# Optimization experiments

Measured on AMD Instinct MI355X. Metric: run time of the kernel, lower is better.

Reference implementation:

```python
import jax, jax.numpy as jnp
import numpy as np

P = 2        # patch size (all 3 dims)
NB = 8       # num_bands
N = 16       # d_state
DTR = 8      # dt_rank = d_model // 16
DCONV = 4    # d_conv
SMAX = 2.0   # smax_dt = smax_B = smax_C


def _ln(x, g, b):
    mu = x.mean(-1, keepdims=True)
    v = ((x - mu) ** 2).mean(-1, keepdims=True)
    return (x - mu) / jnp.sqrt(v + 1e-5) * g + b


def _silu(x):
    return x * jax.nn.sigmoid(x)


def _ssm_layer(x, band, m, rho, Win, bin_, convw, convb, Wx, Wdt, bdt, Alog, Dp,
               Wout, bout, edt, eB, eC, wr, wm):
    # x: [B, L, d_model] -> bidirectional conditioned selective scan (BiFCSSM)
    Bsz, L, _ = x.shape
    ED = convw.shape[0]
    xz = x @ Win + bin_
    xp, z = xz[..., :ED], xz[..., ED:]
    # depthwise causal conv1d over L
    xpad = jnp.pad(xp, ((0, 0), (DCONV - 1, 0), (0, 0)))
    xc = sum(xpad[:, k:k + L, :] * convw[:, k] for k in range(DCONV)) + convb
    xc = _silu(xc)
    dbl = xc @ Wx                                    # [B,L,DTR+2N]
    dt = jax.nn.softplus(dbl[..., :DTR] @ Wdt + bdt)  # [B,L,ED]
    # band/radius/mask conditioned modulation of delta, B, C
    s_dt = SMAX * jax.nn.sigmoid(edt[band][None] + wr[0] * rho[None] + wm[0] * m)
    s_B = SMAX * jax.nn.sigmoid(eB[band][None] + wr[1] * rho[None] + wm[1] * m)
    s_C = SMAX * jax.nn.sigmoid(eC[band][None] + wr[2] * rho[None] + wm[2] * m)
    dt = dt * s_dt[..., None]
    Bm = dbl[..., DTR:DTR + N] * s_B[..., None]       # [B,L,N]
    Cm = dbl[..., DTR + N:] * s_C[..., None]          # [B,L,N]
    A = -jnp.exp(Alog)                                # [ED,N]
    dA = jnp.exp(dt[..., None] * A)                   # [B,L,ED,N]
    dBu = (dA - 1.0) / A * Bm[:, :, None, :] * xc[..., None]   # exact ZOH
    dA_s = jnp.moveaxis(dA, 1, 0)
    dBu_s = jnp.moveaxis(dBu, 1, 0)
    C_s = jnp.moveaxis(Cm, 1, 0)
    h0 = jnp.zeros((Bsz, ED, N), x.dtype)

    def step(h, inp):
        a, bu, c = inp
        h = a * h + bu
        return h, jnp.einsum('ben,bn->be', h, c)

    _, yf = jax.lax.scan(step, h0, (dA_s, dBu_s, C_s))
    _, yb = jax.lax.scan(step, h0, (dA_s, dBu_s, C_s), reverse=True)
    y = jnp.moveaxis(yf + yb, 0, 1) + Dp * xc
    y = y * _silu(z)
    return y @ Wout + bout


def _fwd(kspace_ri, mask, pe_w, pe_b, pu_w, pu_b, ln_g, ln_b, fn_g, fn_b,
         cond_band, cond_rad_w, cond_mask_w, l0_Win, l0_bin, l0_convw, l0_convb,
         l0_Wx, l0_Wdt, l0_bdt, l0_Alog, l0_D, l0_Wout, l0_bout, l0_edt, l0_eB,
         l0_eC, l0_wr, l0_wm):
    Bsz, C, nx, ny, nz = kspace_ri.shape
    gx, gy, gz = nx // P, ny // P, nz // P
    L = gx * gy * gz
    # patch embed (Conv3d, kernel==stride) as blocked einsum
    xr = kspace_ri.reshape(Bsz, C, gx, P, gy, P, gz, P)
    x = jnp.einsum('bcxiyjzk,dcijk->bdxyz', xr, pe_w) + pe_b[None, :, None, None, None]
    DM = x.shape[1]
    x = x.reshape(Bsz, DM, L).transpose(0, 2, 1)               # [B,L,D]
    m = mask.reshape(Bsz, 1, gx, P, gy, P, gz, P).mean(axis=(3, 5, 7)).reshape(Bsz, L)
    m = jnp.clip(m, 0.0, 1.0)
    # raster scan ordering: identity permutation, rho_bar, band ids
    rho = jnp.arange(L, dtype=x.dtype) / float(L - 1)
    band = jnp.clip(jnp.floor(rho * NB).astype(jnp.int32), 0, NB - 1)
    # condition tokens
    cond = cond_band[band][None] + rho[None, :, None] * cond_rad_w + m[:, :, None] * cond_mask_w
    h = _ln(x + cond, ln_g, ln_b)
    h = h + _ssm_layer(_ln(h, fn_g, fn_b), band, m, rho, l0_Win, l0_bin, l0_convw,
                       l0_convb, l0_Wx, l0_Wdt, l0_bdt, l0_Alog, l0_D, l0_Wout,
                       l0_bout, l0_edt, l0_eB, l0_eC, l0_wr, l0_wm)
    # patch unembed (ConvTranspose3d, kernel==stride) as blocked einsum
    hg = h.transpose(0, 2, 1).reshape(Bsz, DM, gx, gy, gz)
    out = jnp.einsum('bdxyz,dcijk->bcxiyjzk', hg, pu_w).reshape(Bsz, C, nx, ny, nz)
    out = out + pu_b[None, :, None, None, None]
    return kspace_ri + out


def setup_inputs() -> dict:
    key = jax.random.key(0)
    ks = jax.random.split(key, 24)
    ED, DM, CIN = 256, 128, 16

    def nrm(k, shape, s):
        return jax.random.normal(k, shape, jnp.float32) * s

    return {
        'kspace_ri': jax.random.normal(ks[0], (1, CIN, 64, 64, 16), jnp.float32),
        'mask': jax.random.uniform(ks[1], (1, 1, 64, 64, 16), jnp.float32),
        'pe_w': nrm(ks[2], (DM, CIN, P, P, P), 0.09),
        'pe_b': nrm(ks[3], (DM,), 0.02),
        'pu_w': nrm(ks[4], (DM, CIN, P, P, P), 0.05),
        'pu_b': jnp.zeros((CIN,), jnp.float32),
        'ln_g': jnp.ones((DM,), jnp.float32),
        'ln_b': jnp.zeros((DM,), jnp.float32),
        'fn_g': jnp.ones((DM,), jnp.float32),
        'fn_b': jnp.zeros((DM,), jnp.float32),
        'cond_band': nrm(ks[5], (NB, DM), 0.02),
        'cond_rad_w': nrm(ks[6], (DM,), 0.02),
        'cond_mask_w': nrm(ks[7], (DM,), 0.02),
        'l0_Win': nrm(ks[8], (DM, 2 * ED), 0.05),
        'l0_bin': jnp.zeros((2 * ED,), jnp.float32),
        'l0_convw': nrm(ks[9], (ED, DCONV), 0.2),
        'l0_convb': jnp.zeros((ED,), jnp.float32),
        'l0_Wx': nrm(ks[10], (ED, DTR + 2 * N), 0.05),
        'l0_Wdt': nrm(ks[11], (DTR, ED), 0.1),
        'l0_bdt': jnp.full((ED,), -3.0, jnp.float32),
        'l0_Alog': jnp.log(jnp.tile(jnp.arange(1, N + 1, dtype=jnp.float32), (ED, 1))),
        'l0_D': jnp.ones((ED,), jnp.float32),
        'l0_Wout': nrm(ks[12], (ED, DM), 0.05),
        'l0_bout': jnp.zeros((DM,), jnp.float32),
        'l0_edt': nrm(ks[13], (NB,), 0.1),
        'l0_eB': nrm(ks[14], (NB,), 0.1),
        'l0_eC': nrm(ks[15], (NB,), 0.1),
        'l0_wr': nrm(ks[16], (3,), 0.1),
        'l0_wm': nrm(ks[17], (3,), 0.1),
    }


def reference(kspace_ri, mask, pe_w, pe_b, pu_w, pu_b, ln_g, ln_b, fn_g, fn_b,
              cond_band, cond_rad_w, cond_mask_w, l0_Win, l0_bin, l0_convw,
              l0_convb, l0_Wx, l0_Wdt, l0_bdt, l0_Alog, l0_D, l0_Wout, l0_bout,
              l0_edt, l0_eB, l0_eC, l0_wr, l0_wm):
    return _fwd(kspace_ri, mask, pe_w, pe_b, pu_w, pu_b, ln_g, ln_b, fn_g, fn_b,
                cond_band, cond_rad_w, cond_mask_w, l0_Win, l0_bin, l0_convw,
                l0_convb, l0_Wx, l0_Wdt, l0_bdt, l0_Alog, l0_D, l0_Wout, l0_bout,
                l0_edt, l0_eB, l0_eC, l0_wr, l0_wm)
```

## Files before the change

### kernel.cpp

```cpp
#include <hip/hip_runtime.h>
#include <hip/hip_bf16.h>

#define L_TOK 8192
#define NCh 512
#define CLh 16
#define NSEG 8
#define CPS (NCh / NSEG)
#define LOG2E 1.44269504088896f

typedef short bf16x8 __attribute__((ext_vector_type(8)));
typedef float f32x4 __attribute__((ext_vector_type(4)));

static __device__ __forceinline__ float nexp2(float x) {
#if __has_builtin(__builtin_amdgcn_exp2f)
    return __builtin_amdgcn_exp2f(x);
#else
    return exp2f(x);
#endif
}
static __device__ __forceinline__ float sigm(float x) {
    return 1.f / (1.f + nexp2(-x * LOG2E));
}
static __device__ __forceinline__ ushort f2bf(float x) {
    union { float f; uint u; } v; v.f = x;
    uint r = v.u + 0x7fffu + ((v.u >> 16) & 1u);
    return (ushort)(r >> 16);
}
static __device__ __forceinline__ float bf2f(ushort h) {
    union { float f; uint u; } v; v.u = ((uint)h) << 16;
    return v.f;
}
static __device__ __forceinline__ void f2hl(float x, ushort* hi, ushort* lo) {
    ushort h = f2bf(x);
    *hi = h;
    *lo = f2bf(x - bf2f(h));
}

#define W_PE   0
#define W_WIN  16384
#define W_WOUT 81920
#define W_PU   114688
#define W_PROJ 131072
#define W_TOT  212992

__global__ __launch_bounds__(256) void embed_ln_k(const float* __restrict__ ks,
                                                  const float* __restrict__ pe_w,
                                                  const float* __restrict__ Win,
                                                  const float* __restrict__ Wx, const float* __restrict__ Wdt,
                                                  const float* __restrict__ Wout, const float* __restrict__ pu_w,
                                                  const float* __restrict__ mask,
                                                  const float* __restrict__ pe_b, const float* __restrict__ cond_band,
                                                  const float* __restrict__ cond_rad, const float* __restrict__ cond_mask,
                                                  const float* __restrict__ ln_g, const float* __restrict__ ln_b,
                                                  const float* __restrict__ fn_g, const float* __restrict__ fn_b,
                                                  ushort* __restrict__ wH, ushort* __restrict__ wL,
                                                  float* __restrict__ mbuf,
                                                  float* __restrict__ h_,
                                                  ushort* __restrict__ hnH, ushort* __restrict__ hnL) {
    const int tid = threadIdx.x;
    if (blockIdx.x >= 512) {
        int b = blockIdx.x - 512;
        if (b >= 832) {
            int l = (b - 832) * 256 + tid;
            int xg = l >> 8, yg = (l >> 3) & 31, zg = l & 7;
            float s = 0.f;
            for (int i2 = 0; i2 < 2; ++i2)
                for (int j2 = 0; j2 < 2; ++j2)
                    for (int k2 = 0; k2 < 2; ++k2)
                        s += mask[(2 * xg + i2) * 1024 + (2 * yg + j2) * 16 + 2 * zg + k2];
            s *= 0.125f;
            mbuf[l] = fminf(fmaxf(s, 0.f), 1.f);
            return;
        }
        int i = b * 256 + tid;
        float v;
        if (i < 16384) {
            v = pe_w[i];
        } else if (i < 81920) {
            int j = i - 16384; int n = j >> 7, k = j & 127;
            v = Win[k * 512 + n];
        } else if (i < 114688) {
            int j = i - 81920; int n = j >> 8, k = j & 255;
            v = Wout[k * 128 + n];
        } else if (i < 131072) {
            int j = i - 114688; int n = j >> 7, k = j & 127;
            v = pu_w[k * 128 + n];
        } else {
            int j = i - 131072; int n = j >> 8, k = j & 255;
            if (n < 256) {
                float s = 0.f;
#pragma unroll
                for (int r = 0; r < 8; ++r) s += Wx[k * 40 + r] * Wdt[r * 256 + n];
                v = s;
            } else if (n < 288) {
                v = Wx[k * 40 + 8 + (n - 256)];
            } else {
                v = 0.f;
            }
        }
        ushort h, lo; f2hl(v, &h, &lo);
        wH[i] = h; wL[i] = lo;
        return;
    }

    __shared__ __align__(16) char smem[50176];
    __shared__ float mpool[16];
    ushort (*AsH)[72] = (ushort(*)[72])(smem);
    ushort (*AsL)[72] = (ushort(*)[72])(smem + 2304);
    ushort (*BsH)[72] = (ushort(*)[72])(smem + 4608);
    ushort (*BsL)[72] = (ushort(*)[72])(smem + 23040);
    float*  ksb       = (float*)(smem + 41472);
    float  (*Cs)[132] = (float(*)[132])(smem);

    const int lane = tid & 63, wn = tid >> 6;
    const int ln = lane & 15, q = lane >> 4;
    const int mb = blockIdx.x * 16;
    const int xg = mb >> 8, yg0 = (mb >> 3) & 31;

    for (int v = tid; v < 512; v += 256) {
        int seg = v >> 2, zq = v & 3;
        int cc = seg >> 3, i2 = (seg >> 2) & 1, yy = seg & 3;
        float4 t4 = *(const float4*)&ks[cc * 65536 + (2 * xg + i2) * 1024 + (2 * yg0 + yy) * 16 + zq * 4];
        int la = seg * 17 + zq * 4;
        ksb[la] = t4.x; ksb[la + 1] = t4.y; ksb[la + 2] = t4.z; ksb[la + 3] = t4.w;
    }
    if (tid < 16) {
        int l = mb + tid;
        int xg2 = l >> 8, yg2 = (l >> 3) & 31, zg2 = l & 7;
        float s = 0.f;
        for (int i2 = 0; i2 < 2; ++i2)
            for (int j2 = 0; j2 < 2; ++j2)
                for (int k2 = 0; k2 < 2; ++k2)
                    s += mask[(2 * xg2 + i2) * 1024 + (2 * yg2 + j2) * 16 + 2 * zg2 + k2];
        mpool[tid] = fminf(fmaxf(s * 0.125f, 0.f), 1.f);
    }

    f32x4 acc[2];
    acc[0] = (f32x4){0.f, 0.f, 0.f, 0.f};
    acc[1] = (f32x4){0.f, 0.f, 0.f, 0.f};

    for (int kc = 0; kc < 128; kc += 64) {
        __syncthreads();
        for (int u = tid; u < 1024; u += 256) {
            int r = u >> 6, kk = u & 63;
            int k = kc + kk;
            int cc = k >> 3, ijk = k & 7;
            int i2 = (ijk >> 2) & 1, j2 = (ijk >> 1) & 1, k2 = ijk & 1;
            int seg = (cc * 2 + i2) * 4 + (r >> 3) * 2 + j2;
            float v = ksb[seg * 17 + (r & 7) * 2 + k2];
            ushort hh, ll; f2hl(v, &hh, &ll);
            AsH[r][kk] = hh; AsL[r][kk] = ll;
        }
        for (int u = tid; u < 1024; u += 256) {
            int n = u >> 3, g = u & 7;
            const float* pw = &pe_w[n * 128 + kc + g * 8];
            float4 p0 = *(const float4*)pw;
            float4 p1 = *(const float4*)(pw + 4);
            union { ushort us[8]; uint4 v4; } hh, ll;
            f2hl(p0.x, &hh.us[0], &ll.us[0]); f2hl(p0.y, &hh.us[1], &ll.us[1]);
            f2hl(p0.z, &hh.us[2], &ll.us[2]); f2hl(p0.w, &hh.us[3], &ll.us[3]);
            f2hl(p1.x, &hh.us[4], &ll.us[4]); f2hl(p1.y, &hh.us[5], &ll.us[5]);
            f2hl(p1.z, &hh.us[6], &ll.us[6]); f2hl(p1.w, &hh.us[7], &ll.us[7]);
            *(uint4*)&BsH[n][g * 8] = hh.v4;
            *(uint4*)&BsL[n][g * 8] = ll.v4;
        }
        __syncthreads();
#pragma unroll
        for (int ks_ = 0; ks_ < 64; ks_ += 32) {
            const int kk = ks_ + q * 8;
            bf16x8 ah = *(const bf16x8*)&AsH[ln][kk];
            bf16x8 al = *(const bf16x8*)&AsL[ln][kk];
#pragma unroll
            for (int cb = 0; cb < 2; ++cb) {
                bf16x8 bh = *(const bf16x8*)&BsH[wn * 32 + cb * 16 + ln][kk];
                bf16x8 bl = *(const bf16x8*)&BsL[wn * 32 + cb * 16 + ln][kk];
                acc[cb] = __builtin_amdgcn_mfma_f32_16x16x32_bf16(ah, bh, acc[cb], 0, 0, 0);
                acc[cb] = __builtin_amdgcn_mfma_f32_16x16x32_bf16(ah, bl, acc[cb], 0, 0, 0);
                acc[cb] = __builtin_amdgcn_mfma_f32_16x16x32_bf16(al, bh, acc[cb], 0, 0, 0);
            }
        }
    }
    __syncthreads();
#pragma unroll
    for (int cb = 0; cb < 2; ++cb) {
#pragma unroll
        for (int r = 0; r < 4; ++r) {
            int row = q * 4 + r;
            int col = wn * 32 + cb * 16 + ln;
            int l = mb + row;
            float rho = (float)l * (1.0f / 8191.0f);
            int band = min(7, (int)(rho * 8.0f));
            Cs[row][col] = acc[cb][r] + pe_b[col] + cond_band[band * 128 + col]
                           + rho * cond_rad[col] + mpool[row] * cond_mask[col];
        }
    }
    __syncthreads();
    {
        int row = tid >> 4, j = tid & 15;
        int l = mb + row;
        float v8[8];
        float s = 0.f, s2 = 0.f;
#pragma unroll
        for (int i = 0; i < 8; ++i) {
            float v = Cs[row][j * 8 + i];
            v8[i] = v; s += v; s2 += v * v;
        }
#pragma unroll
        for (int o = 1; o < 16; o <<= 1) { s += __shfl_xor(s, o, 16); s2 += __shfl_xor(s2, o, 16); }
        float mu = s * (1.f / 128.f);
        float var = s2 * (1.f / 128.f) - mu * mu;
        float rstd = rsqrtf(fmaxf(var, 0.f) + 1e-5f);
        float hv[8];
        s = 0.f; s2 = 0.f;
#pragma unroll
        for (int i = 0; i < 8; ++i) {
            int col = j * 8 + i;
            float h = (v8[i] - mu) * rstd * ln_g[col] + ln_b[col];
            hv[i] = h; s += h; s2 += h * h;
        }
#pragma unroll
        for (int i = 0; i < 8; i += 4)
            *(float4*)&h_[(size_t)l * 128 + j * 8 + i] = make_float4(hv[i], hv[i + 1], hv[i + 2], hv[i + 3]);
#pragma unroll
        for (int o = 1; o < 16; o <<= 1) { s += __shfl_xor(s, o, 16); s2 += __shfl_xor(s2, o, 16); }
        mu = s * (1.f / 128.f);
        var = s2 * (1.f / 128.f) - mu * mu;
        rstd = rsqrtf(fmaxf(var, 0.f) + 1e-5f);
        union { ushort u[8]; uint4 v4; } oh, ol;
#pragma unroll
        for (int i = 0; i < 8; ++i) {
            int col = j * 8 + i;
            float o2 = (hv[i] - mu) * rstd * fn_g[col] + fn_b[col];
            ushort hh, ll; f2hl(o2, &hh, &ll);
            oh.u[i] = hh; ol.u[i] = ll;
        }
        *(uint4*)&hnH[(size_t)l * 128 + j * 8] = oh.v4;
        *(uint4*)&hnL[(size_t)l * 128 + j * 8] = ol.v4;
    }
}

__global__ __launch_bounds__(256) void win_k(const ushort* __restrict__ Ah, const ushort* __restrict__ Al,
                                             const ushort* __restrict__ wH, const ushort* __restrict__ wL,
                                             const float* __restrict__ bin_,
                                             float* __restrict__ xp, float* __restrict__ sz) {
    __shared__ ushort AsH[64][72], AsL[64][72];
    __shared__ ushort BsH[64][72], BsL[64][72];
    const int tid = threadIdx.x;
    const int lane = tid & 63, wave = tid >> 6;
    const int wm = wave & 1, wn = wave >> 1;
    const int ln = lane & 15, q = lane >> 4;
    const int mb = blockIdx.x * 64, nb = blockIdx.y * 64;

    f32x4 acc[2][2];
#pragma unroll
    for (int rb = 0; rb < 2; ++rb)
#pragma unroll
        for (int cb = 0; cb < 2; ++cb) acc[rb][cb] = (f32x4){0.f, 0.f, 0.f, 0.f};

    for (int kc = 0; kc < 128; kc += 64) {
        __syncthreads();
        for (int u = tid; u < 512; u += 256) {
            int r = u >> 3, g = u & 7;
            size_t go = (size_t)(mb + r) * 128 + kc + g * 8;
            *(uint4*)&AsH[r][g * 8] = *(const uint4*)&Ah[go];
            *(uint4*)&AsL[r][g * 8] = *(const uint4*)&Al[go];
        }
        for (int u = tid; u < 512; u += 256) {
            int n = u >> 3, g = u & 7;
            size_t go = (size_t)(W_WIN) + (size_t)(nb + n) * 128 + kc + g * 8;
            *(uint4*)&BsH[n][g * 8] = *(const uint4*)&wH[go];
            *(uint4*)&BsL[n][g * 8] = *(const uint4*)&wL[go];
        }
        __syncthreads();
#pragma unroll
        for (int ks_ = 0; ks_ < 64; ks_ += 32) {
            const int kk = ks_ + q * 8;
            bf16x8 ah[2], al[2], bh[2], bl[2];
#pragma unroll
            for (int rb = 0; rb < 2; ++rb) {
                ah[rb] = *(const bf16x8*)&AsH[wm * 32 + rb * 16 + ln][kk];
                al[rb] = *(const bf16x8*)&AsL[wm * 32 + rb * 16 + ln][kk];
            }
#pragma unroll
            for (int cb = 0; cb < 2; ++cb) {
                bh[cb] = *(const bf16x8*)&BsH[wn * 32 + cb * 16 + ln][kk];
                bl[cb] = *(const bf16x8*)&BsL[wn * 32 + cb * 16 + ln][kk];
            }
#pragma unroll
            for (int rb = 0; rb < 2; ++rb)
#pragma unroll
                for (int cb = 0; cb < 2; ++cb) {
                    acc[rb][cb] = __builtin_amdgcn_mfma_f32_16x16x32_bf16(ah[rb], bh[cb], acc[rb][cb], 0, 0, 0);
                    acc[rb][cb] = __builtin_amdgcn_mfma_f32_16x16x32_bf16(ah[rb], bl[cb], acc[rb][cb], 0, 0, 0);
                    acc[rb][cb] = __builtin_amdgcn_mfma_f32_16x16x32_bf16(al[rb], bh[cb], acc[rb][cb], 0, 0, 0);
                }
        }
    }
#pragma unroll
    for (int rb = 0; rb < 2; ++rb)
#pragma unroll
        for (int cb = 0; cb < 2; ++cb)
#pragma unroll
            for (int r = 0; r < 4; ++r) {
                int l = mb + wm * 32 + rb * 16 + q * 4 + r;
                int col = nb + wn * 32 + cb * 16 + ln;
                float v = acc[rb][cb][r] + bin_[col];
                if (col < 256) {
                    xp[(size_t)l * 256 + col] = v;
                } else {
                    sz[(size_t)l * 256 + (col - 256)] = v * sigm(v);
                }
            }
}

__global__ __launch_bounds__(512) void proj_k(const float* __restrict__ xp,
                                              const float* __restrict__ convw, const float* __restrict__ convb,
                                              const ushort* __restrict__ wH, const ushort* __restrict__ wL,
                                              const float* __restrict__ bdt, const float* __restrict__ mbuf,
                                              const float* __restrict__ edt, const float* __restrict__ eB,
                                              const float* __restrict__ eC, const float* __restrict__ wr,
                                              const float* __restrict__ wm,
                                              float* __restrict__ xc, float* __restrict__ dt,
                                              float* __restrict__ Bm, float* __restrict__ Cm) {
    __shared__ __align__(16) char smem[52224];
    ushort (*AsH)[264] = (ushort(*)[264])(smem);
    ushort (*AsL)[264] = (ushort(*)[264])(smem + 16896);
    ushort (*BsH)[72]  = (ushort(*)[72])(smem + 33792);
    ushort (*BsL)[72]  = (ushort(*)[72])(smem + 43008);
    const int tid = threadIdx.x;
    const int mb = blockIdx.x * 32;

    {
        const int cg = tid & 63;
        const int rg = tid >> 6;
        const int c0 = cg * 4;
        float4 cb4 = *(const float4*)&convb[c0];
        float4 cw0 = *(const float4*)&convw[(c0 + 0) * 4];
        float4 cw1 = *(const float4*)&convw[(c0 + 1) * 4];
        float4 cw2 = *(const float4*)&convw[(c0 + 2) * 4];
        float4 cw3 = *(const float4*)&convw[(c0 + 3) * 4];
        const int lbase = mb + rg * 4;
        float4 zero = make_float4(0.f, 0.f, 0.f, 0.f);
        float4 x0 = (lbase - 3 >= 0) ? *(const float4*)&xp[(size_t)(lbase - 3) * 256 + c0] : zero;
        float4 x1 = (lbase - 2 >= 0) ? *(const float4*)&xp[(size_t)(lbase - 2) * 256 + c0] : zero;
        float4 x2 = (lbase - 1 >= 0) ? *(const float4*)&xp[(size_t)(lbase - 1) * 256 + c0] : zero;
#pragma unroll
        for (int rr = 0; rr < 4; ++rr) {
            int l = lbase + rr;
            float4 x3 = *(const float4*)&xp[(size_t)l * 256 + c0];
            float o0 = cb4.x + x0.x * cw0.x + x1.x * cw0.y + x2.x * cw0.z + x3.x * cw0.w;
            float o1 = cb4.y + x0.y * cw1.x + x1.y * cw1.y + x2.y * cw1.z + x3.y * cw1.w;
            float o2 = cb4.z + x0.z * cw2.x + x1.z * cw2.y + x2.z * cw2.z + x3.z * cw2.w;
            float o3 = cb4.w + x0.w * cw3.x + x1.w * cw3.y + x2.w * cw3.z + x3.w * cw3.w;
            o0 *= sigm(o0); o1 *= sigm(o1); o2 *= sigm(o2); o3 *= sigm(o3);
            *(float4*)&xc[(size_t)l * 256 + c0] = make_float4(o0, o1, o2, o3);
            union { ushort u[4]; uint2 v2; } hh, ll;
            f2hl(o0, &hh.u[0], &ll.u[0]); f2hl(o1, &hh.u[1], &ll.u[1]);
            f2hl(o2, &hh.u[2], &ll.u[2]); f2hl(o3, &hh.u[3], &ll.u[3]);
            int row = l - mb;
            *(uint2*)&AsH[row][c0] = hh.v2;
            *(uint2*)&AsL[row][c0] = ll.v2;
            x0 = x1; x1 = x2; x2 = x3;
        }
    }
    const int pn = tid >> 3, pg = tid & 7;
    uint4 regH = *(const uint4*)&wH[(size_t)W_PROJ + (size_t)pn * 256 + pg * 8];
    uint4 regL = *(const uint4*)&wL[(size_t)W_PROJ + (size_t)pn * 256 + pg * 8];
    __syncthreads();

    const int lane = tid & 63, wave = tid >> 6;
    const int wm2 = wave & 1, wn4 = wave >> 1;
    const int ln = lane & 15, q = lane >> 4;
    for (int it = 0; it < 5; ++it) {
        int nb = it * 64;
        f32x4 acc = (f32x4){0.f, 0.f, 0.f, 0.f};
        for (int kci = 0; kci < 4; ++kci) {
            int kc = kci * 64;
            __syncthreads();
            *(uint4*)&BsH[pn][pg * 8] = regH;
            *(uint4*)&BsL[pn][pg * 8] = regL;
            int s = it * 4 + kci;
            if (s < 19) {
                int s2 = s + 1;
                int nb2 = (s2 >> 2) * 64, kc2 = (s2 & 3) * 64;
                size_t go = (size_t)W_PROJ + (size_t)(nb2 + pn) * 256 + kc2 + pg * 8;
                regH = *(const uint4*)&wH[go];
                regL = *(const uint4*)&wL[go];
            }
            __syncthreads();
#pragma unroll
            for (int ks_ = 0; ks_ < 64; ks_ += 32) {
                const int kka = kc + ks_ + q * 8;
                const int kkb = ks_ + q * 8;
                bf16x8 ah = *(const bf16x8*)&AsH[wm2 * 16 + ln][kka];
                bf16x8 al = *(const bf16x8*)&AsL[wm2 * 16 + ln][kka];
                bf16x8 bh = *(const bf16x8*)&BsH[wn4 * 16 + ln][kkb];
                bf16x8 bl = *(const bf16x8*)&BsL[wn4 * 16 + ln][kkb];
                acc = __builtin_amdgcn_mfma_f32_16x16x32_bf16(ah, bh, acc, 0, 0, 0);
                acc = __builtin_amdgcn_mfma_f32_16x16x32_bf16(ah, bl, acc, 0, 0, 0);
                acc = __builtin_amdgcn_mfma_f32_16x16x32_bf16(al, bh, acc, 0, 0, 0);
            }
        }
#pragma unroll
        for (int r = 0; r < 4; ++r) {
            int l = mb + wm2 * 16 + q * 4 + r;
            int col = nb + wn4 * 16 + ln;
            float v = acc[r];
            float rho = (float)l * (1.0f / 8191.0f);
            int band = min(7, (int)(rho * 8.0f));
            float mv = mbuf[l];
            if (col < 256) {
                float sc0 = 2.0f * sigm(edt[band] + wr[0] * rho + wm[0] * mv);
                float v2 = v + bdt[col];
                float sp = (v2 > 20.f) ? v2 : log1pf(expf(v2));
                dt[(size_t)l * 256 + col] = sp * sc0;
            } else if (col < 272) {
                float sc1 = 2.0f * sigm(eB[band] + wr[1] * rho + wm[1] * mv);
                Bm[(size_t)l * 16 + (col - 256)] = v * sc1;
            } else if (col < 288) {
                float sc2 = 2.0f * sigm(eC[band] + wr[2] * rho + wm[2] * mv);
                Cm[(size_t)l * 16 + (col - 272)] = v * sc2;
            }
        }
    }
}

__global__ __launch_bounds__(512) void scan0_k(const float* __restrict__ dt, const float* __restrict__ xc,
                                               const float* __restrict__ Bm, const float* __restrict__ Alog,
                                               float* __restrict__ Hb, float* __restrict__ sdtb) {
    const int c = blockIdx.x;
    const int tid = threadIdx.x;
    const int dir = tid >> 8, e = tid & 255;
    __shared__ float bms[CLh][16];
    for (int idx = tid; idx < CLh * 16; idx += 512)
        bms[idx >> 4][idx & 15] = Bm[c * (CLh * 16) + idx];
    float A2[16], iv[16], h[16];
#pragma unroll
    for (int n = 0; n < 16; ++n) {
        float ea = nexp2(Alog[e * 16 + n] * LOG2E);
        A2[n] = -ea * LOG2E;
        iv[n] = -1.0f / ea;
        h[n] = 0.f;
    }
    const int base = c * CLh;
    float cu[8], cx[8], nu[8], nx[8];
#pragma unroll
    for (int j = 0; j < 8; ++j) {
        int p = dir ? (CLh - 1 - j) : j;
        cu[j] = dt[(size_t)(base + p) * 256 + e];
        cx[j] = xc[(size_t)(base + p) * 256 + e];
    }
    __syncthreads();
    float sdt = 0.f;
#pragma unroll
    for (int g = 0; g < CLh / 8; ++g) {
        if (g + 1 < CLh / 8) {
#pragma unroll
            for (int j = 0; j < 8; ++j) {
                int s = (g + 1) * 8 + j;
                int p = dir ? (CLh - 1 - s) : s;
                nu[j] = dt[(size_t)(base + p) * 256 + e];
                nx[j] = xc[(size_t)(base + p) * 256 + e];
            }
        }
#pragma unroll
        for (int j = 0; j < 8; ++j) {
            float u = cu[j], xv = cx[j];
            int s = g * 8 + j;
            int p = dir ? (CLh - 1 - s) : s;
            union { float4 v[4]; float f[16]; } bb;
            const float4* bp = (const float4*)&bms[p][0];
            bb.v[0] = bp[0]; bb.v[1] = bp[1]; bb.v[2] = bp[2]; bb.v[3] = bp[3];
#pragma unroll
            for (int n = 0; n < 16; ++n) {
                float a = nexp2(A2[n] * u);
                float w = xv * bb.f[n] * iv[n];
                h[n] = a * (h[n] + w) - w;
            }
            sdt += u;
        }
#pragma unroll
        for (int j = 0; j < 8; ++j) { cu[j] = nu[j]; cx[j] = nx[j]; }
    }
    const size_t hofs = (size_t)(dir * NCh + c) * 4096 + e * 16;
#pragma unroll
    for (int j = 0; j < 4; ++j)
        *(float4*)&Hb[hofs + 4 * j] = make_float4(h[4 * j], h[4 * j + 1], h[4 * j + 2], h[4 * j + 3]);
    if (dir == 0) sdtb[c * 256 + e] = sdt;
}

__global__ __launch_bounds__(256) void combine1_k(const float* __restrict__ Hb, const float* __restrict__ sdtb,
                                                  const float* __restrict__ Alog,
                                                  float* __restrict__ Hpp, float* __restrict__ cumsdtb,
                                                  float* __restrict__ segq, float* __restrict__ segsdt) {
    const int gid = blockIdx.x * 256 + threadIdx.x;
    const int seg = gid >> 13;
    const int r = gid & 8191;
    const int d1 = r >> 12, en = r & 4095, e1 = en >> 4;
    const float A2e = -nexp2(Alog[en] * LOG2E) * LOG2E;
    float hi = 0.f, cum = 0.f;
    for (int k = 0; k < CPS; ++k) {
        const int pos = seg * CPS + k;
        const int c2 = d1 ? (NCh - 1 - pos) : pos;
        const size_t o2 = (size_t)(d1 * NCh + c2) * 4096 + en;
        const float sv = sdtb[c2 * 256 + e1];
        Hpp[o2] = hi;
        if ((en & 15) == 0) cumsdtb[(d1 * NCh + c2) * 256 + e1] = cum;
        hi = nexp2(A2e * sv) * hi + Hb[o2];
        cum += sv;
    }
    segq[(d1 * NSEG + seg) * 4096 + en] = hi;
    if ((en & 15) == 0) segsdt[(d1 * NSEG + seg) * 256 + e1] = cum;
}

__global__ __launch_bounds__(64) void combine2_k(const float* __restrict__ segq, const float* __restrict__ segsdt,
                                                 const float* __restrict__ Alog, float* __restrict__ segpre) {
    const int gid = blockIdx.x * 64 + threadIdx.x;
    const int d1 = gid >> 12, en = gid & 4095, e1 = en >> 4;
    const float A2e = -nexp2(Alog[en] * LOG2E) * LOG2E;
    float hi = 0.f;
#pragma unroll
    for (int s = 0; s < NSEG; ++s) {
        segpre[(d1 * NSEG + s) * 4096 + en] = hi;
        hi = nexp2(A2e * segsdt[(d1 * NSEG + s) * 256 + e1]) * hi + segq[(d1 * NSEG + s) * 4096 + en];
    }
}

template <int DIR>
static __device__ __forceinline__ void scan_dir(const float* __restrict__ dt, const float* __restrict__ xc,
                                                int base, int e,
                                                const float (*bms)[16], const float (*cms)[16],
                                                const float* A2, const float* iv,
                                                float* h, float* yreg, float* cxl) {
    float cu[8], cx[8], nu[8], nx[8];
#pragma unroll
    for (int j = 0; j < 8; ++j) {
        const int p = DIR ? (CLh - 1 - j) : j;
        cu[j] = dt[(size_t)(base + p) * 256 + e];
        cx[j] = xc[(size_t)(base + p) * 256 + e];
    }
#pragma unroll
    for (int g = 0; g < CLh / 8; ++g) {
        if (g + 1 < CLh / 8) {
#pragma unroll
            for (int j = 0; j < 8; ++j) {
                const int s = (g + 1) * 8 + j;
                const int p = DIR ? (CLh - 1 - s) : s;
                nu[j] = dt[(size_t)(base + p) * 256 + e];
                nx[j] = xc[(size_t)(base + p) * 256 + e];
            }
        }
#pragma unroll
        for (int j = 0; j < 8; ++j) {
            const int s = g * 8 + j;
            const int p = DIR ? (CLh - 1 - s) : s;
            float u = cu[j], xv = cx[j];
            union { float4 v[4]; float f[16]; } bb, cc;
            const float4* bp = (const float4*)&bms[p][0];
            bb.v[0] = bp[0]; bb.v[1] = bp[1]; bb.v[2] = bp[2]; bb.v[3] = bp[3];
            const float4* cp = (const float4*)&cms[p][0];
            cc.v[0] = cp[0]; cc.v[1] = cp[1]; cc.v[2] = cp[2]; cc.v[3] = cp[3];
            float y = 0.f;
#pragma unroll
            for (int n = 0; n < 16; ++n) {
                float a = nexp2(A2[n] * u);
                float w = xv * bb.f[n] * iv[n];
                h[n] = a * (h[n] + w) - w;
                y += h[n] * cc.f[n];
            }
            yreg[p] = y;
        }
#pragma unroll
        for (int j = 0; j < 8; ++j) { cu[j] = nu[j]; cx[j] = nx[j]; }
    }
#pragma unroll
    for (int j = 0; j < 8; ++j) cxl[j] = cx[j];
}

__global__ __launch_bounds__(512) void scan1g_k(const float* __restrict__ dt, const float* __restrict__ xc,
                                                const float* __restrict__ Bm, const float* __restrict__ Cm,
                                                const float* __restrict__ Alog,
                                                const float* __restrict__ Hpp, const float* __restrict__ cumsdtb,
                                                const float* __restrict__ segpre,
                                                const float* __restrict__ sz, const float* __restrict__ Dp,
                                                ushort* __restrict__ AHo, ushort* __restrict__ ALo) {
    const int c = blockIdx.x;
    const int tid = threadIdx.x;
    const int dir = tid >> 8;
    const int e = tid & 255;
    __shared__ float bms[CLh][16];
    __shared__ float cms[CLh][16];
    __shared__ float ysF[8][256];
    __shared__ float ysB[8][256];
    for (int idx = tid; idx < CLh * 16; idx += 512) {
        bms[idx >> 4][idx & 15] = Bm[c * (CLh * 16) + idx];
        cms[idx >> 4][idx & 15] = Cm[c * (CLh * 16) + idx];
    }
    float A2[16], iv[16], h[16];
#pragma unroll
    for (int n = 0; n < 16; ++n) {
        float ea = nexp2(Alog[e * 16 + n] * LOG2E);
        A2[n] = -ea * LOG2E;
        iv[n] = -1.0f / ea;
    }
    {
        const int pos = dir ? (NCh - 1 - c) : c;
        const int seg = pos / CPS;
        const float cum = cumsdtb[(dir * NCh + c) * 256 + e];
        const size_t hofs = (size_t)(dir * NCh + c) * 4096 + e * 16;
        const size_t so = (size_t)(dir * NSEG + seg) * 4096 + e * 16;
#pragma unroll
        for (int jj = 0; jj < 4; ++jj) {
            float4 hv = *(const float4*)&Hpp[hofs + 4 * jj];
            float4 sv = *(const float4*)&segpre[so + 4 * jj];
            h[4 * jj + 0] = hv.x + nexp2(A2[4 * jj + 0] * cum) * sv.x;
            h[4 * jj + 1] = hv.y + nexp2(A2[4 * jj + 1] * cum) * sv.y;
            h[4 * jj + 2] = hv.z + nexp2(A2[4 * jj + 2] * cum) * sv.z;
            h[4 * jj + 3] = hv.w + nexp2(A2[4 * jj + 3] * cum) * sv.w;
        }
    }
    const int base = c * CLh;
    float yreg[CLh], cxl[8];
    __syncthreads();
    if (dir == 0) {
        scan_dir<0>(dt, xc, base, e, bms, cms, A2, iv, h, yreg, cxl);
#pragma unroll
        for (int j = 0; j < 8; ++j) ysF[j][e] = yreg[j];
    } else {
        scan_dir<1>(dt, xc, base, e, bms, cms, A2, iv, h, yreg, cxl);
#pragma unroll
        for (int j = 0; j < 8; ++j) ysB[j][e] = yreg[8 + j];
    }
    __syncthreads();
    const float dpv = Dp[e];
    if (dir == 0) {
#pragma unroll
        for (int j = 0; j < 8; ++j) {
            const int l = 8 + j;
            size_t gl = (size_t)(base + l) * 256 + e;
            float a = (yreg[l] + ysB[j][e] + dpv * cxl[j]) * sz[gl];
            ushort hh, ll; f2hl(a, &hh, &ll);
            AHo[gl] = hh; ALo[gl] = ll;
        }
    } else {
#pragma unroll
        for (int j = 0; j < 8; ++j) {
            const int l = 7 - j;
            size_t gl = (size_t)(base + l) * 256 + e;
            float a = (ysF[l][e] + yreg[l] + dpv * cxl[j]) * sz[gl];
            ushort hh, ll; f2hl(a, &hh, &ll);
            AHo[gl] = hh; ALo[gl] = ll;
        }
    }
}

__global__ __launch_bounds__(512) void wu_k(const ushort* __restrict__ AH, const ushort* __restrict__ AL,
                                            const ushort* __restrict__ wH, const ushort* __restrict__ wL,
                                            const float* __restrict__ bout, const float* __restrict__ h_,
                                            const float* __restrict__ pu_b, const float* __restrict__ ks,
                                            float* __restrict__ out) {
    __shared__ __align__(16) char smem[70656];
    ushort (*AsH)[264] = (ushort(*)[264])(smem);
    ushort (*AsL)[264] = (ushort(*)[264])(smem + 16896);
    ushort (*BsH)[72]  = (ushort(*)[72])(smem + 33792);
    ushort (*BsL)[72]  = (ushort(*)[72])(smem + 52224);
    ushort (*hfH)[136] = (ushort(*)[136])(smem);
    ushort (*hfL)[136] = (ushort(*)[136])(smem + 8704);

    const int tid = threadIdx.x;
    const int lane = tid & 63, wave = tid >> 6;
    const int wm = wave & 1, wn = wave >> 1;
    const int ln = lane & 15, q = lane >> 4;
    const int mb = blockIdx.x * 32;

    for (int u = tid; u < 1024; u += 512) {
        int r = u >> 5, g = u & 31;
        size_t go = (size_t)(mb + r) * 256 + g * 8;
        *(uint4*)&AsH[r][g * 8] = *(const uint4*)&AH[go];
        *(uint4*)&AsL[r][g * 8] = *(const uint4*)&AL[go];
    }

    f32x4 acc[2];
    acc[0] = (f32x4){0.f, 0.f, 0.f, 0.f};
    acc[1] = (f32x4){0.f, 0.f, 0.f, 0.f};

    for (int kc = 0; kc < 256; kc += 64) {
        __syncthreads();
        for (int u = tid; u < 1024; u += 512) {
            int n = u >> 3, g = u & 7;
            size_t go = (size_t)(W_WOUT) + (size_t)n * 256 + kc + g * 8;
            *(uint4*)&BsH[n][g * 8] = *(const uint4*)&wH[go];
            *(uint4*)&BsL[n][g * 8] = *(const uint4*)&wL[go];
        }
        __syncthreads();
#pragma unroll
        for (int ks_ = 0; ks_ < 64; ks_ += 32) {
            const int kka = kc + ks_ + q * 8;
            const int kkb = ks_ + q * 8;
            bf16x8 ah = *(const bf16x8*)&AsH[wm * 16 + ln][kka];
            bf16x8 al = *(const bf16x8*)&AsL[wm * 16 + ln][kka];
#pragma unroll
            for (int cb = 0; cb < 2; ++cb) {
                bf16x8 bh = *(const bf16x8*)&BsH[wn * 32 + cb * 16 + ln][kkb];
                bf16x8 bl = *(const bf16x8*)&BsL[wn * 32 + cb * 16 + ln][kkb];
                acc[cb] = __builtin_amdgcn_mfma_f32_16x16x32_bf16(ah, bh, acc[cb], 0, 0, 0);
                acc[cb] = __builtin_amdgcn_mfma_f32_16x16x32_bf16(ah, bl, acc[cb], 0, 0, 0);
                acc[cb] = __builtin_amdgcn_mfma_f32_16x16x32_bf16(al, bh, acc[cb], 0, 0, 0);
            }
        }
    }
    __syncthreads();
#pragma unroll
    for (int cb = 0; cb < 2; ++cb)
#pragma unroll
        for (int r = 0; r < 4; ++r) {
            int row = wm * 16 + q * 4 + r;
            int col = wn * 32 + cb * 16 + ln;
            float v = acc[cb][r] + bout[col] + h_[(size_t)(mb + row) * 128 + col];
            ushort hh, ll; f2hl(v, &hh, &ll);
            hfH[row][col] = hh;
            hfL[row][col] = ll;
        }
    __syncthreads();

    f32x4 acc2[2];
    acc2[0] = (f32x4){0.f, 0.f, 0.f, 0.f};
    acc2[1] = (f32x4){0.f, 0.f, 0.f, 0.f};
    for (int kc = 0; kc < 128; kc += 64) {
        __syncthreads();
        for (int u = tid; u < 1024; u += 512) {
            int n = u >> 3, g = u & 7;
            size_t go = (size_t)(W_PU) + (size_t)n * 128 + kc + g * 8;
            *(uint4*)&BsH[n][g * 8] = *(const uint4*)&wH[go];
            *(uint4*)&BsL[n][g * 8] = *(const uint4*)&wL[go];
        }
        __syncthreads();
#pragma unroll
        for (int ks_ = 0; ks_ < 64; ks_ += 32) {
            const int kka = kc + ks_ + q * 8;
            const int kkb = ks_ + q * 8;
            bf16x8 ah = *(const bf16x8*)&hfH[wm * 16 + ln][kka];
            bf16x8 al = *(const bf16x8*)&hfL[wm * 16 + ln][kka];
#pragma unroll
            for (int cb = 0; cb < 2; ++cb) {
                bf16x8 bh = *(const bf16x8*)&BsH[wn * 32 + cb * 16 + ln][kkb];
                bf16x8 bl = *(const bf16x8*)&BsL[wn * 32 + cb * 16 + ln][kkb];
                acc2[cb] = __builtin_amdgcn_mfma_f32_16x16x32_bf16(ah, bh, acc2[cb], 0, 0, 0);
                acc2[cb] = __builtin_amdgcn_mfma_f32_16x16x32_bf16(ah, bl, acc2[cb], 0, 0, 0);
                acc2[cb] = __builtin_amdgcn_mfma_f32_16x16x32_bf16(al, bh, acc2[cb], 0, 0, 0);
            }
        }
    }
#pragma unroll
    for (int cb = 0; cb < 2; ++cb)
#pragma unroll
        for (int r = 0; r < 4; ++r) {
            int l = mb + wm * 16 + q * 4 + r;
            int col = wn * 32 + cb * 16 + ln;
            int xg = l >> 8, yg = (l >> 3) & 31, zg = l & 7;
            int cch = col >> 3, ijk = col & 7;
            int i2 = (ijk >> 2) & 1, j2 = (ijk >> 1) & 1, k2 = ijk & 1;
            size_t idx = (size_t)((cch * 64 + 2 * xg + i2) * 64 + (2 * yg + j2)) * 16 + 2 * zg + k2;
            out[idx] = acc2[cb][r] + pu_b[cch] + ks[idx];
        }
}

extern "C" void kernel_launch(void* const* d_in, const int* in_sizes, int n_in,
                              void* d_out, int out_size, void* d_ws, size_t ws_size,
                              hipStream_t stream) {
    const float* ks    = (const float*)d_in[0];
    const float* mask  = (const float*)d_in[1];
    const float* pe_w  = (const float*)d_in[2];
    const float* pe_b  = (const float*)d_in[3];
    const float* pu_w  = (const float*)d_in[4];
    const float* pu_b  = (const float*)d_in[5];
    const float* ln_g  = (const float*)d_in[6];
    const float* ln_b  = (const float*)d_in[7];
    const float* fn_g  = (const float*)d_in[8];
    const float* fn_b  = (const float*)d_in[9];
    const float* cond_band = (const float*)d_in[10];
    const float* cond_rad  = (const float*)d_in[11];
    const float* cond_mask = (const float*)d_in[12];
    const float* Win   = (const float*)d_in[13];
    const float* bin_  = (const float*)d_in[14];
    const float* convw = (const float*)d_in[15];
    const float* convb = (const float*)d_in[16];
    const float* Wx    = (const float*)d_in[17];
    const float* Wdt   = (const float*)d_in[18];
    const float* bdt   = (const float*)d_in[19];
    const float* Alog  = (const float*)d_in[20];
    const float* Dp    = (const float*)d_in[21];
    const float* Wout  = (const float*)d_in[22];
    const float* bout  = (const float*)d_in[23];
    const float* edt   = (const float*)d_in[24];
    const float* eB    = (const float*)d_in[25];
    const float* eC    = (const float*)d_in[26];
    const float* wr    = (const float*)d_in[27];
    const float* wm    = (const float*)d_in[28];
    float* out = (float*)d_out;

    char* base = (char*)d_ws;
    size_t o = 0;
    auto alloc = [&](size_t bytes) { char* p = base + o; o += (bytes + 255) & ~(size_t)255; return p; };
    float*  mbuf = (float*)alloc(32768);
    ushort* wH   = (ushort*)alloc(W_TOT * 2);
    ushort* wL   = (ushort*)alloc(W_TOT * 2);
    float*  h_   = (float*)alloc(4194304);
    ushort* hnH  = (ushort*)alloc(2097152);
    ushort* hnL  = (ushort*)alloc(2097152);
    float*  xp   = (float*)alloc(8388608);
    float*  sz   = (float*)alloc(8388608);
    float*  xc   = (float*)alloc(8388608);
    float*  dt   = (float*)alloc(8388608);
    float*  Bm   = (float*)alloc(524288);
    float*  Cm   = (float*)alloc(524288);
    float*  Hb   = (float*)alloc((size_t)2 * NCh * 4096 * 4);
    float*  Hpp  = (float*)alloc((size_t)2 * NCh * 4096 * 4);
    float*  sdtb = (float*)alloc((size_t)NCh * 256 * 4);
    float*  cumsdtb = (float*)alloc((size_t)2 * NCh * 256 * 4);
    float*  segq    = (float*)alloc((size_t)2 * NSEG * 4096 * 4);
    float*  segsdt  = (float*)alloc((size_t)2 * NSEG * 256 * 4);
    float*  segpre  = (float*)alloc((size_t)2 * NSEG * 4096 * 4);
    ushort* AHo  = (ushort*)alloc(4194304);
    ushort* ALo  = (ushort*)alloc(4194304);

    embed_ln_k<<<1376, 256, 0, stream>>>(ks, pe_w, Win, Wx, Wdt, Wout, pu_w, mask,
                                         pe_b, cond_band, cond_rad, cond_mask,
                                         ln_g, ln_b, fn_g, fn_b,
                                         wH, wL, mbuf, h_, hnH, hnL);
    win_k<<<dim3(128, 8), 256, 0, stream>>>(hnH, hnL, wH, wL, bin_, xp, sz);
    proj_k<<<256, 512, 0, stream>>>(xp, convw, convb, wH, wL, bdt, mbuf, edt, eB, eC, wr, wm,
                                    xc, dt, Bm, Cm);
    scan0_k<<<NCh, 512, 0, stream>>>(dt, xc, Bm, Alog, Hb, sdtb);
    combine1_k<<<256, 256, 0, stream>>>(Hb, sdtb, Alog, Hpp, cumsdtb, segq, segsdt);
    combine2_k<<<128, 64, 0, stream>>>(segq, segsdt, Alog, segpre);
    scan1g_k<<<NCh, 512, 0, stream>>>(dt, xc, Bm, Cm, Alog, Hpp, cumsdtb, segpre, sz, Dp, AHo, ALo);
    wu_k<<<256, 512, 0, stream>>>(AHo, ALo, wH, wL, bout, h_, pu_b, ks, out);
}
```

Measured before the change: 272.6 us.

## Compute local scan outputs in first pass and apply carry-in correction separately

The first chunk scan now also produces per-token local outputs y and cumulative dt sums and writes them to global buffers. The second chunk rescan is replaced by a fully parallel per-token kernel that adds the carry-in state contribution, C·exp(A·S)·h_prev, instead of re-running the recurrence. This removes the duplicated sequential scan work. In exchange it writes and reads two extra 16 MB buffers and recomputes exponentials for both directions per token.

After: 284.1 us. +4.2%, slower.

```diff
diff --git a/kernel.cpp b/kernel.cpp
--- a/kernel.cpp
+++ b/kernel.cpp
@@ -425,15 +425,20 @@
     }
 }
 
-__global__ __launch_bounds__(512) void scan0_k(const float* __restrict__ dt, const float* __restrict__ xc,
-                                               const float* __restrict__ Bm, const float* __restrict__ Alog,
-                                               float* __restrict__ Hb, float* __restrict__ sdtb) {
+__global__ __launch_bounds__(512) void scan0y_k(const float* __restrict__ dt, const float* __restrict__ xc,
+                                                const float* __restrict__ Bm, const float* __restrict__ Cm,
+                                                const float* __restrict__ Alog,
+                                                float* __restrict__ Hb, float* __restrict__ sdtb,
+                                                float* __restrict__ ybuf, float* __restrict__ sbuf) {
     const int c = blockIdx.x;
     const int tid = threadIdx.x;
     const int dir = tid >> 8, e = tid & 255;
     __shared__ float bms[CLh][16];
-    for (int idx = tid; idx < CLh * 16; idx += 512)
+    __shared__ float cms[CLh][16];
+    for (int idx = tid; idx < CLh * 16; idx += 512) {
         bms[idx >> 4][idx & 15] = Bm[c * (CLh * 16) + idx];
+        cms[idx >> 4][idx & 15] = Cm[c * (CLh * 16) + idx];
+    }
     float A2[16], iv[16], h[16];
 #pragma unroll
     for (int n = 0; n < 16; ++n) {
@@ -468,16 +473,23 @@
             float u = cu[j], xv = cx[j];
             int s = g * 8 + j;
             int p = dir ? (CLh - 1 - s) : s;
-            union { float4 v[4]; float f[16]; } bb;
+            union { float4 v[4]; float f[16]; } bb, cc;
             const float4* bp = (const float4*)&bms[p][0];
             bb.v[0] = bp[0]; bb.v[1] = bp[1]; bb.v[2] = bp[2]; bb.v[3] = bp[3];
+            const float4* cp = (const float4*)&cms[p][0];
+            cc.v[0] = cp[0]; cc.v[1] = cp[1]; cc.v[2] = cp[2]; cc.v[3] = cp[3];
+            float y = 0.f;
 #pragma unroll
             for (int n = 0; n < 16; ++n) {
                 float a = nexp2(A2[n] * u);
                 float w = xv * bb.f[n] * iv[n];
                 h[n] = a * (h[n] + w) - w;
+                y += h[n] * cc.f[n];
             }
             sdt += u;
+            size_t go = (size_t)(dir * L_TOK + base + p) * 256 + e;
+            ybuf[go] = y;
+            sbuf[go] = sdt;
         }
 #pragma unroll
         for (int j = 0; j < 8; ++j) { cu[j] = nu[j]; cx[j] = nx[j]; }
@@ -526,132 +538,57 @@
     }
 }
 
-template <int DIR>
-static __device__ __forceinline__ void scan_dir(const float* __restrict__ dt, const float* __restrict__ xc,
-                                                int base, int e,
-                                                const float (*bms)[16], const float (*cms)[16],
-                                                const float* A2, const float* iv,
-                                                float* h, float* yreg, float* cxl) {
-    float cu[8], cx[8], nu[8], nx[8];
-#pragma unroll
-    for (int j = 0; j < 8; ++j) {
-        const int p = DIR ? (CLh - 1 - j) : j;
-        cu[j] = dt[(size_t)(base + p) * 256 + e];
-        cx[j] = xc[(size_t)(base + p) * 256 + e];
-    }
-#pragma unroll
-    for (int g = 0; g < CLh / 8; ++g) {
-        if (g + 1 < CLh / 8) {
-#pragma unroll
-            for (int j = 0; j < 8; ++j) {
-                const int s = (g + 1) * 8 + j;
-                const int p = DIR ? (CLh - 1 - s) : s;
-                nu[j] = dt[(size_t)(base + p) * 256 + e];
-                nx[j] = xc[(size_t)(base + p) * 256 + e];
-            }
-        }
-#pragma unroll
-        for (int j = 0; j < 8; ++j) {
-            const int s = g * 8 + j;
-            const int p = DIR ? (CLh - 1 - s) : s;
-            float u = cu[j], xv = cx[j];
-            union { float4 v[4]; float f[16]; } bb, cc;
-            const float4* bp = (const float4*)&bms[p][0];
-            bb.v[0] = bp[0]; bb.v[1] = bp[1]; bb.v[2] = bp[2]; bb.v[3] = bp[3];
-            const float4* cp = (const float4*)&cms[p][0];
-            cc.v[0] = cp[0]; cc.v[1] = cp[1]; cc.v[2] = cp[2]; cc.v[3] = cp[3];
-            float y = 0.f;
-#pragma unroll
-            for (int n = 0; n < 16; ++n) {
-                float a = nexp2(A2[n] * u);
-                float w = xv * bb.f[n] * iv[n];
-                h[n] = a * (h[n] + w) - w;
-                y += h[n] * cc.f[n];
-            }
-            yreg[p] = y;
-        }
-#pragma unroll
-        for (int j = 0; j < 8; ++j) { cu[j] = nu[j]; cx[j] = nx[j]; }
-    }
-#pragma unroll
-    for (int j = 0; j < 8; ++j) cxl[j] = cx[j];
-}
-
-__global__ __launch_bounds__(512) void scan1g_k(const float* __restrict__ dt, const float* __restrict__ xc,
-                                                const float* __restrict__ Bm, const float* __restrict__ Cm,
-                                                const float* __restrict__ Alog,
-                                                const float* __restrict__ Hpp, const float* __restrict__ cumsdtb,
-                                                const float* __restrict__ segpre,
-                                                const float* __restrict__ sz, const float* __restrict__ Dp,
-                                                ushort* __restrict__ AHo, ushort* __restrict__ ALo) {
-    const int c = blockIdx.x;
-    const int tid = threadIdx.x;
-    const int dir = tid >> 8;
-    const int e = tid & 255;
-    __shared__ float bms[CLh][16];
-    __shared__ float cms[CLh][16];
-    __shared__ float ysF[8][256];
-    __shared__ float ysB[8][256];
-    for (int idx = tid; idx < CLh * 16; idx += 512) {
-        bms[idx >> 4][idx & 15] = Bm[c * (CLh * 16) + idx];
-        cms[idx >> 4][idx & 15] = Cm[c * (CLh * 16) + idx];
-    }
-    float A2[16], iv[16], h[16];
-#pragma unroll
-    for (int n = 0; n < 16; ++n) {
-        float ea = nexp2(Alog[e * 16 + n] * LOG2E);
-        A2[n] = -ea * LOG2E;
-        iv[n] = -1.0f / ea;
-    }
-    {
+__global__ __launch_bounds__(512) void final_k(const float* __restrict__ ybuf, const float* __restrict__ sbuf,
+                                               const float* __restrict__ xc, const float* __restrict__ sz,
+                                               const float* __restrict__ Cm, const float* __restrict__ Alog,
+                                               const float* __restrict__ Hpp, const float* __restrict__ cumsdtb,
+                                               const float* __restrict__ segpre, const float* __restrict__ Dp,
+                                               ushort* __restrict__ AHo, ushort* __restrict__ ALo) {
+    const int gid = blockIdx.x * 512 + threadIdx.x;
+    const int l = gid >> 8, e = gid & 255;
+    const int c = l >> 4;
+    union { float4 v[4]; float f[16]; } A2, cmv;
+#pragma unroll
+    for (int j = 0; j < 4; ++j) {
+        float4 av = *(const float4*)&Alog[e * 16 + 4 * j];
+        A2.f[4 * j + 0] = -nexp2(av.x * LOG2E) * LOG2E;
+        A2.f[4 * j + 1] = -nexp2(av.y * LOG2E) * LOG2E;
+        A2.f[4 * j + 2] = -nexp2(av.z * LOG2E) * LOG2E;
+        A2.f[4 * j + 3] = -nexp2(av.w * LOG2E) * LOG2E;
+        cmv.v[j] = *(const float4*)&Cm[l * 16 + 4 * j];
+    }
+    float corr[2];
+#pragma unroll
+    for (int dir = 0; dir < 2; ++dir) {
+        const int cidx = dir * NCh + c;
         const int pos = dir ? (NCh - 1 - c) : c;
         const int seg = pos / CPS;
-        const float cum = cumsdtb[(dir * NCh + c) * 256 + e];
-        const size_t hofs = (size_t)(dir * NCh + c) * 4096 + e * 16;
+        const float cum = cumsdtb[cidx * 256 + e];
+        const size_t hofs = (size_t)cidx * 4096 + e * 16;
         const size_t so = (size_t)(dir * NSEG + seg) * 4096 + e * 16;
-#pragma unroll
-        for (int jj = 0; jj < 4; ++jj) {
-            float4 hv = *(const float4*)&Hpp[hofs + 4 * jj];
-            float4 sv = *(const float4*)&segpre[so + 4 * jj];
-            h[4 * jj + 0] = hv.x + nexp2(A2[4 * jj + 0] * cum) * sv.x;
-            h[4 * jj + 1] = hv.y + nexp2(A2[4 * jj + 1] * cum) * sv.y;
-            h[4 * jj + 2] = hv.z + nexp2(A2[4 * jj + 2] * cum) * sv.z;
-            h[4 * jj + 3] = hv.w + nexp2(A2[4 * jj + 3] * cum) * sv.w;
-        }
-    }
-    const int base = c * CLh;
-    float yreg[CLh], cxl[8];
-    __syncthreads();
-    if (dir == 0) {
-        scan_dir<0>(dt, xc, base, e, bms, cms, A2, iv, h, yreg, cxl);
-#pragma unroll
-        for (int j = 0; j < 8; ++j) ysF[j][e] = yreg[j];
-    } else {
-        scan_dir<1>(dt, xc, base, e, bms, cms, A2, iv, h, yreg, cxl);
-#pragma unroll
-        for (int j = 0; j < 8; ++j) ysB[j][e] = yreg[8 + j];
-    }
-    __syncthreads();
-    const float dpv = Dp[e];
-    if (dir == 0) {
-#pragma unroll
-        for (int j = 0; j < 8; ++j) {
-            const int l = 8 + j;
-            size_t gl = (size_t)(base + l) * 256 + e;
-            float a = (yreg[l] + ysB[j][e] + dpv * cxl[j]) * sz[gl];
-            ushort hh, ll; f2hl(a, &hh, &ll);
-            AHo[gl] = hh; ALo[gl] = ll;
-        }
-    } else {
-#pragma unroll
-        for (int j = 0; j < 8; ++j) {
-            const int l = 7 - j;
-            size_t gl = (size_t)(base + l) * 256 + e;
-            float a = (ysF[l][e] + yreg[l] + dpv * cxl[j]) * sz[gl];
-            ushort hh, ll; f2hl(a, &hh, &ll);
-            AHo[gl] = hh; ALo[gl] = ll;
-        }
-    }
+        const float S = sbuf[(size_t)(dir * L_TOK + l) * 256 + e];
+        float acc = 0.f;
+#pragma unroll
+        for (int j = 0; j < 4; ++j) {
+            float4 hv = *(const float4*)&Hpp[hofs + 4 * j];
+            float4 sv = *(const float4*)&segpre[so + 4 * j];
+            float hp0 = hv.x + nexp2(A2.f[4 * j + 0] * cum) * sv.x;
+            float hp1 = hv.y + nexp2(A2.f[4 * j + 1] * cum) * sv.y;
+            float hp2 = hv.z + nexp2(A2.f[4 * j + 2] * cum) * sv.z;
+            float hp3 = hv.w + nexp2(A2.f[4 * j + 3] * cum) * sv.w;
+            acc += cmv.f[4 * j + 0] * nexp2(A2.f[4 * j + 0] * S) * hp0;
+            acc += cmv.f[4 * j + 1] * nexp2(A2.f[4 * j + 1] * S) * hp1;
+            acc += cmv.f[4 * j + 2] * nexp2(A2.f[4 * j + 2] * S) * hp2;
+            acc += cmv.f[4 * j + 3] * nexp2(A2.f[4 * j + 3] * S) * hp3;
+        }
+        corr[dir] = acc;
+    }
+    const size_t gl = (size_t)l * 256 + e;
+    float yF = ybuf[gl] + corr[0];
+    float yB = ybuf[(size_t)L_TOK * 256 + gl] + corr[1];
+    float a = (yF + yB + Dp[e] * xc[gl]) * sz[gl];
+    ushort hh, ll; f2hl(a, &hh, &ll);
+    AHo[gl] = hh; ALo[gl] = ll;
 }
 
 __global__ __launch_bounds__(512) void wu_k(const ushort* __restrict__ AH, const ushort* __restrict__ AL,
@@ -821,6 +758,8 @@
     float*  segq    = (float*)alloc((size_t)2 * NSEG * 4096 * 4);
     float*  segsdt  = (float*)alloc((size_t)2 * NSEG * 256 * 4);
     float*  segpre  = (float*)alloc((size_t)2 * NSEG * 4096 * 4);
+    float*  ybuf = (float*)alloc((size_t)2 * L_TOK * 256 * 4);
+    float*  sbuf = (float*)alloc((size_t)2 * L_TOK * 256 * 4);
     ushort* AHo  = (ushort*)alloc(4194304);
     ushort* ALo  = (ushort*)alloc(4194304);
 
@@ -831,9 +770,10 @@
     win_k<<<dim3(128, 8), 256, 0, stream>>>(hnH, hnL, wH, wL, bin_, xp, sz);
     proj_k<<<256, 512, 0, stream>>>(xp, convw, convb, wH, wL, bdt, mbuf, edt, eB, eC, wr, wm,
                                     xc, dt, Bm, Cm);
-    scan0_k<<<NCh, 512, 0, stream>>>(dt, xc, Bm, Alog, Hb, sdtb);
+    scan0y_k<<<NCh, 512, 0, stream>>>(dt, xc, Bm, Cm, Alog, Hb, sdtb, ybuf, sbuf);
     combine1_k<<<256, 256, 0, stream>>>(Hb, sdtb, Alog, Hpp, cumsdtb, segq, segsdt);
     combine2_k<<<128, 64, 0, stream>>>(segq, segsdt, Alog, segpre);
-    scan1g_k<<<NCh, 512, 0, stream>>>(dt, xc, Bm, Cm, Alog, Hpp, cumsdtb, segpre, sz, Dp, AHo, ALo);
+    final_k<<<4096, 512, 0, stream>>>(ybuf, sbuf, xc, sz, Cm, Alog, Hpp, cumsdtb, segpre, Dp,
+                                      AHo, ALo);
     wu_k<<<256, 512, 0, stream>>>(AHo, ALo, wH, wL, bout, h_, pu_b, ks, out);
 }
```
